# Kernel tuning notes

Measured on AMD Instinct MI355X. Metric: run time of the kernel, lower is better.

Reference implementation:

```python
import jax, jax.numpy as jnp
import numpy as np

N_SAMPLES = 2 ** 15            # 32768
N_FRAMES = N_SAMPLES // 256    # 128 (window 512, step 256)
N_EVENTS = 8
N_HARM = 8
TOTAL_COEFFS = N_SAMPLES // 2 + 1
NOISE_SPEC = 16
NYQUIST = 22050.0 / 2.0
MAX_F = 3000.0 / NYQUIST
MIN_F = 20.0 / NYQUIST
F_SPAN = MAX_F - MIN_F
Y = 20 + NOISE_SPEC + N_FRAMES + N_HARM   # 172
DIM = Y + 128 + 128                        # 428
BATCH = 16


def lin_interp(x, out_size):
    # torch F.interpolate(mode='linear', align_corners=False) along last dim
    n = x.shape[-1]
    scale = n / out_size
    coords = jnp.clip((jnp.arange(out_size) + 0.5) * scale - 0.5, 0.0, n - 1.0)
    lo = jnp.floor(coords).astype(jnp.int32)
    hi = jnp.minimum(lo + 1, n - 1)
    w = (coords - lo).astype(x.dtype)
    return x[..., lo] * (1.0 - w) + x[..., hi] * w


def setup_inputs() -> dict:
    key = jax.random.key(0)
    k1, k2 = jax.random.split(key)
    x = jax.random.normal(k1, (BATCH, N_EVENTS, DIM), dtype=jnp.float32)
    noise = jax.random.uniform(k2, (BATCH, N_EVENTS, N_SAMPLES), dtype=jnp.float32)
    return {"x": x, "noise": noise}


def reference(x, noise):
    B = x.shape[0]
    x = jax.nn.sigmoid(x)
    means = x[..., 0:1]
    stds = x[..., 1:2] * 0.1
    amps = x[..., 2:3] ** 2
    f0 = x[..., 3:4] ** 2
    factors = 1.0 + x[..., 4:12] * 7.0
    mags = (x[..., 12:20] * 0.9999) ** 2
    noise_coeff = x[..., 20:20 + NOISE_SPEC]
    fine_env = x[..., 36:36 + N_FRAMES] * 2.0 - 1.0
    amp_factors = x[..., 164:172] ** 2
    f0_var = x[..., 172:300]

    # fine amplitude envelope: cumsum over frames, clamp, upsample
    fe = jnp.clip(jnp.cumsum(fine_env.reshape(-1, N_FRAMES), axis=-1), 0.0, 1.0)
    fe = lin_interp(fe, N_SAMPLES).reshape(B, N_EVENTS, N_SAMPLES)

    # localized band-limited noise, gaussian time window
    rng = jnp.arange(N_SAMPLES, dtype=x.dtype)
    mu = jnp.clip(means * N_SAMPLES, -(N_SAMPLES // 2), N_SAMPLES * 1.5)
    sigma = jnp.clip((1e-8 + stds) * N_SAMPLES, 0.0, N_SAMPLES - 1.0)
    z = (rng - mu) / sigma                                   # (B,E,S)
    probs = jnp.exp(-0.5 * z * z) / (sigma * np.sqrt(2.0 * np.pi))
    probs = probs / (jnp.max(jnp.abs(probs), axis=-1, keepdims=True) + 1e-12)
    u = noise * 2.0 - 1.0                                    # uniform(-1,1)
    spec_shape = lin_interp(noise_coeff, TOTAL_COEFFS)       # (B,E,total_coeffs)
    ns = jnp.fft.rfft(u, axis=-1, norm='ortho') * spec_shape
    nz = jnp.fft.irfft(ns, n=N_SAMPLES, axis=-1, norm='ortho')
    atoms = probs * nz * amps * fe                           # (B,E,S)

    # harmonic resonance
    f0f = f0.reshape(-1, 1)                                  # (BE,1)
    var = f0_var.reshape(-1, N_FRAMES) * (f0f * 0.01)        # (BE,F)
    f0t = lin_interp(f0f + var, N_SAMPLES)                   # (BE,S)
    f0t = MIN_F + f0t * F_SPAN
    f0t = jnp.where(f0t > 1.0, 0.0, f0t)
    fac = factors.reshape(-1, N_HARM).at[:, 0].set(1.0)      # (BE,H)
    freqs = f0t[:, None, :] * fac[:, :, None] * np.pi        # (BE,H,S)
    osc = jnp.sin(jnp.cumsum(freqs, axis=-1)) * amp_factors.reshape(-1, N_HARM, 1)
    # cumprod of a constant per frame == geometric powers
    mg = mags.reshape(-1, N_HARM, 1) ** jnp.arange(1, N_FRAMES + 1, dtype=x.dtype)
    mg = lin_interp(mg, N_SAMPLES)                           # (BE,H,S)
    res = jnp.sum(osc * mg, axis=1).reshape(B, N_EVENTS, N_SAMPLES)

    # fft convolution (zero-padded to 2S to avoid circular wrap)
    pa = jnp.pad(atoms, ((0, 0), (0, 0), (0, N_SAMPLES)))
    pr = jnp.pad(res, ((0, 0), (0, 0), (0, N_SAMPLES)))
    conv = jnp.fft.irfft(jnp.fft.rfft(pa, axis=-1) * jnp.fft.rfft(pr, axis=-1),
                         n=2 * N_SAMPLES, axis=-1)[..., :N_SAMPLES]
    return jnp.sum(conv, axis=1, keepdims=True)              # (B,1,S)
```

## Files before the change

kernel.cpp:

```cpp
#include <hip/hip_runtime.h>
#include <math.h>

#define NSAMP 32768
#define NFFT2 65536
#define NFRM 128
#define PSTRIDE 2688
#define P_FEPAIR 64
#define P_PW2 320
#define P_LQ 1344
#define P_AF 1604
#define P_END 2636
#define TWO_PI_F 6.28318530717958647692f

typedef float2 cplx;

__device__ __forceinline__ cplx cmul_(cplx a, cplx b){ return make_float2(a.x*b.x - a.y*b.y, a.x*b.y + a.y*b.x); }
__device__ __forceinline__ cplx cadd_(cplx a, cplx b){ return make_float2(a.x+b.x, a.y+b.y); }
__device__ __forceinline__ cplx csub_(cplx a, cplx b){ return make_float2(a.x-b.x, a.y-b.y); }

__device__ __forceinline__ unsigned int packbf2(float re, float im){
  unsigned int ur = __float_as_uint(re);
  unsigned int ui = __float_as_uint(im);
  ur = (ur + 0x7FFFu + ((ur>>16)&1u)) >> 16;
  ui = (ui + 0x7FFFu + ((ui>>16)&1u)) & 0xFFFF0000u;
  return ur | ui;
}

template<bool INV>
__device__ __forceinline__ void dft4_(cplx x0,cplx x1,cplx x2,cplx x3, cplx&y0,cplx&y1,cplx&y2,cplx&y3){
  cplx t0=cadd_(x0,x2), t1=csub_(x0,x2), t2=cadd_(x1,x3), t3=csub_(x1,x3);
  y0=cadd_(t0,t2); y2=csub_(t0,t2);
  cplx it3 = make_float2(-t3.y, t3.x);
  if (INV){ y1=cadd_(t1,it3); y3=csub_(t1,it3); }
  else    { y1=csub_(t1,it3); y3=cadd_(t1,it3); }
}

template<bool INV>
__device__ __forceinline__ void dft8ip_(cplx* v){
  cplx e0,e1,e2,e3,o0,o1,o2,o3;
  dft4_<INV>(v[0],v[2],v[4],v[6], e0,e1,e2,e3);
  dft4_<INV>(v[1],v[3],v[5],v[7], o0,o1,o2,o3);
  const float r = 0.70710678118654752440f;
  cplx w1 = INV ? make_float2(r, r)    : make_float2(r,-r);
  cplx w2 = INV ? make_float2(0.f,1.f) : make_float2(0.f,-1.f);
  cplx w3 = INV ? make_float2(-r,r)    : make_float2(-r,-r);
  cplx t1 = cmul_(o1,w1), t2 = cmul_(o2,w2), t3 = cmul_(o3,w3);
  v[0]=cadd_(e0,o0); v[4]=csub_(e0,o0);
  v[1]=cadd_(e1,t1); v[5]=csub_(e1,t1);
  v[2]=cadd_(e2,t2); v[6]=csub_(e2,t2);
  v[3]=cadd_(e3,t3); v[7]=csub_(e3,t3);
}

template<bool INV>
__device__ __forceinline__ void dft16ip_(cplx* v){
  cplx t0[4], t1[4], t2[4], t3[4];
  dft4_<INV>(v[0], v[4], v[8],  v[12], t0[0],t0[1],t0[2],t0[3]);
  dft4_<INV>(v[1], v[5], v[9],  v[13], t1[0],t1[1],t1[2],t1[3]);
  dft4_<INV>(v[2], v[6], v[10], v[14], t2[0],t2[1],t2[2],t2[3]);
  dft4_<INV>(v[3], v[7], v[11], v[15], t3[0],t3[1],t3[2],t3[3]);
  const float C1=0.92387953251128675613f, S1=0.38268343236508977172f, R2=0.70710678118654752440f;
  #define TWD_(x, cc, ss) (INV ? cmul_((x), make_float2((cc), (ss))) : cmul_((x), make_float2((cc), -(ss))))
  t1[1] = TWD_(t1[1], C1, S1);
  t1[2] = TWD_(t1[2], R2, R2);
  t1[3] = TWD_(t1[3], S1, C1);
  t2[1] = TWD_(t2[1], R2, R2);
  t2[2] = TWD_(t2[2], 0.f, 1.f);
  t2[3] = TWD_(t2[3], -R2, R2);
  t3[1] = TWD_(t3[1], S1, C1);
  t3[2] = TWD_(t3[2], -R2, R2);
  t3[3] = TWD_(t3[3], -C1, -S1);
  #undef TWD_
  dft4_<INV>(t0[0], t1[0], t2[0], t3[0], v[0], v[4], v[8],  v[12]);
  dft4_<INV>(t0[1], t1[1], t2[1], t3[1], v[1], v[5], v[9],  v[13]);
  dft4_<INV>(t0[2], t1[2], t2[2], t3[2], v[2], v[6], v[10], v[14]);
  dft4_<INV>(t0[3], t1[3], t2[3], t3[3], v[3], v[7], v[11], v[15]);
}

template<int R0, bool INV>
__device__ __forceinline__ void fft_core(float* lre, float* lim, int t){
  constexpr int Q = R0/16;
  constexpr int S1 = R0 + 8;
  int g = t >> 4, a = t & 15;
  cplx v[Q];
  #pragma unroll
  for (int bb=0;bb<Q;bb++){ int idx = g*S1 + a + 16*bb; v[bb]=make_float2(lre[idx],lim[idx]); }
  if constexpr (Q==16) dft16ip_<INV>(v); else dft8ip_<INV>(v);
  float th = (INV?TWO_PI_F:-TWO_PI_F)*(float)a/(float)R0;
  float sn,cs; __sincosf(th,&sn,&cs);
  cplx w1=make_float2(cs,sn), wu=w1;
  #pragma unroll
  for (int c=1;c<Q;c++){ v[c]=cmul_(v[c],wu); wu=cmul_(wu,w1); }
  __syncthreads();
  #pragma unroll
  for (int c=0;c<Q;c++){ int m = a*Q + ((c+a)&(Q-1)); lre[g*S1+m]=v[c].x; lim[g*S1+m]=v[c].y; }
  __syncthreads();
}

template<int R0, bool INV>
__device__ __forceinline__ bool fft_stage2(const float* lre, const float* lim, int t, int& g2, int& c2, cplx* z){
  constexpr int Q = R0/16; constexpr int S1 = R0+8;
  bool active = (R0==256) || (t < 16*Q);
  g2 = (R0==256)?(t>>4):(t>>3);
  c2 = (R0==256)?(t&15):(t&7);
  if (active){
    #pragma unroll
    for (int a2=0;a2<16;a2++){ int m = a2*Q + ((c2+a2)&(Q-1)); z[a2]=make_float2(lre[g2*S1+m], lim[g2*S1+m]); }
    dft16ip_<INV>(z);
  }
  return active;
}

__global__ __launch_bounds__(256) void k_fft_pack_fwd1(const float* __restrict__ noise, cplx* __restrict__ dst, float interBase){
  constexpr int Q=16, S1=264;
  __shared__ float lre[4352], lim[4352];
  int t=threadIdx.x;
  int bx=blockIdx.x;
  int sig = bx>>3;
  int tBase=(bx&7)*16;
  const float* n0 = noise + (size_t)(2*sig)*NSAMP;
  const float* n1 = noise + (size_t)(2*sig+1)*NSAMP;
  #pragma unroll
  for (int i=0;i<16;i++){
    int e=t+256*i, g=e&15, r=e>>4;
    int ts = tBase+g+128*r;
    lre[g*S1+r]=n0[ts]*2.f-1.f;
    lim[g*S1+r]=n1[ts]*2.f-1.f;
  }
  __syncthreads();
  fft_core<256,false>(lre,lim,t);
  int g2,c2; cplx z[16];
  fft_stage2<256,false>(lre,lim,t,g2,c2,z);
  int p=tBase+g2;
  float thp=interBase*(float)p;
  float snc,csc; __sincosf(thp*(float)c2,&snc,&csc);
  float sns,css; __sincosf(thp*(float)Q,&sns,&css);
  cplx wu=make_float2(csc,snc), ws=make_float2(css,sns);
  cplx* db = dst + (size_t)sig*NSAMP;
  size_t ob=(size_t)256*(size_t)p+(size_t)c2;
  #pragma unroll
  for (int d=0;d<16;d++){ db[ob+(size_t)(d*16)]=cmul_(z[d],wu); wu=cmul_(wu,ws); }
}

__device__ __forceinline__ void fft128_natural(float* re, float* im, int t){
  __syncthreads();
  fft_core<128,false>(re,im,t);
  int g2,c2; cplx z[16];
  bool act = fft_stage2<128,false>(re,im,t,g2,c2,z);
  __syncthreads();
  if (act){
    #pragma unroll
    for (int d=0;d<16;d++){ int u=c2+8*d; re[u*17+g2]=z[d].x; im[u*17+g2]=z[d].y; }
  }
  __syncthreads();
}

__global__ __launch_bounds__(256) void k_nfilter_ip1(const cplx* __restrict__ src, cplx* __restrict__ dst,
    const float* __restrict__ P){
  __shared__ float aRe[2176], aIm[2176], bRe[2176], bIm[2176];
  __shared__ float fRe[2176], fIm[2176];
  __shared__ float c1s[16], c2sh[16];
  int t=threadIdx.x, pb=blockIdx.x, j=blockIdx.y;
  const cplx* sb = src + ((size_t)j<<15);
  cplx* db = dst + ((size_t)j<<15);
  if (t<16) c1s[t] = P[(size_t)(2*j)*PSTRIDE+28+t];
  else if (t<32) c2sh[t-16] = P[(size_t)(2*j+1)*PSTRIDE+28+(t-16)];
  #pragma unroll
  for (int i=0;i<8;i++){
    int e=t+256*i, g=e&15, r=e>>4;
    int col = (pb<8)? (pb*16+g) : (g*16);
    cplx v = sb[col + (r<<8)];
    aRe[g*136+r]=v.x; aIm[g*136+r]=v.y;
  }
  fft128_natural(aRe,aIm,t);
  if (pb<8){
    #pragma unroll
    for (int i=0;i<8;i++){
      int e=t+256*i, g=e&15, r=e>>4;
      int col = 240-pb*16+g;
      cplx v = sb[col + (r<<8)];
      bRe[g*136+r]=v.x; bIm[g*136+r]=v.y;
    }
    fft128_natural(bRe,bIm,t);
  }
  const float inv32768 = 1.0f/32768.0f;
  if (pb<8){
    for (int s=0;s<2;s++){
      __syncthreads();
      #pragma unroll
      for (int uu=0; uu<8; uu++){
        int g=t&15, u=(t>>4)+16*uu;
        if (g!=0){
          int colK = s? (240-pb*16+g) : (pb*16+g);
          int gm=16-g, um=127-u;
          float Zkx,Zky,Zmx,Zmy;
          if (s==0){ Zkx=aRe[u*17+g]; Zky=aIm[u*17+g]; Zmx=bRe[um*17+gm]; Zmy=bIm[um*17+gm]; }
          else     { Zkx=bRe[u*17+g]; Zky=bIm[u*17+g]; Zmx=aRe[um*17+gm]; Zmy=aIm[um*17+gm]; }
          int k = colK + (u<<8);
          int kb = min(k, NSAMP-k);
          float coords=fminf(fmaxf((kb+0.5f)*(16.0f/16385.0f)-0.5f,0.0f),15.0f);
          int lo=(int)coords; float w=coords-lo; int hi=min(lo+1,15);
          float s1=(c1s[lo]+w*(c1s[hi]-c1s[lo]))*inv32768;
          float s2=(c2sh[lo]+w*(c2sh[hi]-c2sh[lo]))*inv32768;
          float U1x=0.5f*(Zkx+Zmx), U1y=0.5f*(Zky-Zmy);
          float U2x=0.5f*(Zky+Zmy), U2y=-0.5f*(Zkx-Zmx);
          fRe[g*136+u]=U1x*s1 - U2y*s2; fIm[g*136+u]=U1y*s1 + U2x*s2;
        }
      }
      __syncthreads();
      fft_core<128,true>(fRe,fIm,t);
      int gg,cc; cplx z[16];
      bool act = fft_stage2<128,true>(fRe,fIm,t,gg,cc,z);
      if (act && gg!=0){
        int p = (s==0) ? (pb*16+gg) : (240-pb*16+gg);
        float thp=(TWO_PI_F/32768.0f)*(float)p;
        float snc,csc; __sincosf(thp*(float)cc,&snc,&csc);
        float sns,css; __sincosf(thp*8.0f,&sns,&css);
        cplx wu=make_float2(csc,snc), wsx=make_float2(css,sns);
        int ob=128*p+cc;
        #pragma unroll
        for (int d=0;d<16;d++){ db[ob+8*d]=cmul_(z[d],wu); wu=cmul_(wu,wsx); }
      }
    }
  } else {
    __syncthreads();
    #pragma unroll
    for (int uu=0; uu<8; uu++){
      int g=t&15, u=(t>>4)+16*uu;
      int k = g*16 + (u<<8);
      int gm=(16-g)&15;
      int um=(g==0)? ((128-u)&127) : (127-u);
      float Zkx=aRe[u*17+g], Zky=aIm[u*17+g];
      float Zmx=aRe[um*17+gm], Zmy=aIm[um*17+gm];
      int kb = min(k, NSAMP-k);
      float coords=fminf(fmaxf((kb+0.5f)*(16.0f/16385.0f)-0.5f,0.0f),15.0f);
      int lo=(int)coords; float w=coords-lo; int hi=min(lo+1,15);
      float s1=(c1s[lo]+w*(c1s[hi]-c1s[lo]))*inv32768;
      float s2=(c2sh[lo]+w*(c2sh[hi]-c2sh[lo]))*inv32768;
      float U1x=0.5f*(Zkx+Zmx), U1y=0.5f*(Zky-Zmy);
      float U2x=0.5f*(Zky+Zmy), U2y=-0.5f*(Zkx-Zmx);
      fRe[g*136+u]=U1x*s1 - U2y*s2; fIm[g*136+u]=U1y*s1 + U2x*s2;
    }
    __syncthreads();
    fft_core<128,true>(fRe,fIm,t);
    int gg,cc; cplx z[16];
    bool act = fft_stage2<128,true>(fRe,fIm,t,gg,cc,z);
    if (act){
      int p = 16*gg;
      float thp=(TWO_PI_F/32768.0f)*(float)p;
      float snc,csc; __sincosf(thp*(float)cc,&snc,&csc);
      float sns,css; __sincosf(thp*8.0f,&sns,&css);
      cplx wu=make_float2(csc,snc), wsx=make_float2(css,sns);
      int ob=128*p+cc;
      #pragma unroll
      for (int d=0;d<16;d++){ db[ob+8*d]=cmul_(z[d],wu); wu=cmul_(wu,wsx); }
    }
  }
}

__global__ __launch_bounds__(256) void k_ifinal_split(const cplx* __restrict__ src, float* __restrict__ dstf){
  constexpr int S1=264;
  __shared__ float lre[4352], lim[4352];
  int t=threadIdx.x; int bx=blockIdx.x;
  int sig=bx>>3; int tBase=(bx&7)*16;
  const cplx* sb = src + (size_t)sig*NSAMP;
  #pragma unroll
  for (int i=0;i<16;i++){
    int e=t+256*i, g=e&15, r=e>>4;
    cplx vv = sb[tBase+g + (size_t)r*128];
    lre[g*S1+r]=vv.x; lim[g*S1+r]=vv.y;
  }
  __syncthreads();
  fft_core<256,true>(lre,lim,t);
  int g2,c2; cplx z[16];
  fft_stage2<256,true>(lre,lim,t,g2,c2,z);
  __syncthreads();
  #pragma unroll
  for (int d=0;d<16;d++){ int u=c2+16*d; lre[u*17+g2]=z[d].x; lim[u*17+g2]=z[d].y; }
  __syncthreads();
  float* p0 = dstf + (size_t)(2*sig)*NSAMP;
  float* p1 = dstf + (size_t)(2*sig+1)*NSAMP;
  #pragma unroll
  for (int i=0;i<16;i++){
    int e=t+256*i, g3=e&15, u=e>>4;
    int ts = tBase+g3+u*128;
    p0[ts]=lre[u*17+g3]; p1[ts]=lim[u*17+g3];
  }
}

__global__ __launch_bounds__(256) void k_conv_build_fwd1(const float* __restrict__ P,
    const float* __restrict__ NZf, unsigned int* __restrict__ dst, int rowBase, float interBase){
  constexpr int Q=16, S1=264;
  __shared__ float smem[8448];
  float* lre = smem;
  float* lim = smem + 4224;
  float* sTab = smem;
  int t=threadIdx.x;
  int row = rowBase + blockIdx.y;
  int tBase = blockIdx.x*16;
  const float* Pr = P + (size_t)row*PSTRIDE;
  for (int i=t; i<P_END; i+=256) sTab[i] = Pr[i];
  __syncthreads();
  float mu=sTab[0], sigma=sTab[1], amp=sTab[2], pscale=sTab[3];
  float fac[8], mh[8];
  #pragma unroll
  for (int h=0;h<8;h++){ fac[h]=sTab[4+h]; mh[h]=sTab[12+h]; }
  const float2* fe2 = (const float2*)&sTab[P_FEPAIR];
  const float*  pw2 = &sTab[P_PW2];
  const float2* LQt = (const float2*)&sTab[P_LQ];
  const float*  Af  = &sTab[P_AF];
  const float* nzrow = NZf + (size_t)row*NSAMP;
  float vre[8], vim[8];
  #pragma unroll
  for (int i=0;i<8;i++){
    int e=t+256*i, g=e&15, r=e>>4;
    int ts = tBase + g + (r<<8);
    float cc=fminf(fmaxf((ts+0.5f)*(1.0f/256.0f)-0.5f,0.0f),127.0f);
    int lo=(int)cc; float w=cc-lo;
    float2 fp = fe2[lo];
    float fev = fp.x + w*fp.y;
    int slot, n0;
    if (ts<128){ slot=0; n0=ts+1; } else { int km=(ts-128)>>8; slot=km+1; n0=ts-127-(km<<8); }
    float nf=(float)n0, nf2=nf*nf;
    float2 lq = LQt[slot];
    float base = nf*lq.x + nf2*lq.y;
    float wm = (lo<127)? w : 0.0f;
    float resv=0.f;
    #pragma unroll
    for (int h=0;h<8;h++){
      float mgb = pw2[h*128+lo];
      if (mgb > 1e-7f){
        float rr = Af[slot*8+h] + fac[h]*base;
        float fr = rr - floorf(rr);
        float s = __builtin_amdgcn_sinf(fr);
        resv += s*mgb*(1.0f + wm*(mh[h]-1.0f));
      }
    }
    float zz=((float)ts-mu)/sigma;
    float prb=pscale*__expf(-0.5f*zz*zz);
    vre[i] = prb*nzrow[ts]*amp*fev;
    vim[i] = resv;
  }
  __syncthreads();
  #pragma unroll
  for (int i=0;i<8;i++){
    int e=t+256*i, g=e&15, r=e>>4;
    lre[g*S1+r]=vre[i]; lim[g*S1+r]=vim[i];
  }
  #pragma unroll
  for (int i=8;i<16;i++){
    int e=t+256*i, g=e&15, r=e>>4;
    lre[g*S1+r]=0.f; lim[g*S1+r]=0.f;
  }
  __syncthreads();
  fft_core<256,false>(lre,lim,t);
  int g2,c2; cplx z[16];
  fft_stage2<256,false>(lre,lim,t,g2,c2,z);
  int p = tBase+g2;
  float thp = interBase*(float)p;
  float snc,csc; __sincosf(thp*(float)c2,&snc,&csc);
  float sns,css; __sincosf(thp*(float)Q,&sns,&css);
  cplx wu=make_float2(csc,snc), ws=make_float2(css,sns);
  unsigned int* db = dst + (size_t)blockIdx.y*NFFT2;
  size_t ob=(size_t)256*(size_t)p+(size_t)c2;
  #pragma unroll
  for (int d=0; d<16; d++){
    cplx val = cmul_(z[d],wu);
    db[ob+(size_t)(d*16)] = packbf2(val.x, val.y);
    wu=cmul_(wu,ws);
  }
}

__global__ __launch_bounds__(256) void k_sq_inv1(const unsigned int* __restrict__ C,
    cplx* __restrict__ E0, cplx* __restrict__ E1){
  constexpr int Q=16, S1=264;
  __shared__ float lre[4352], lim[4352];
  int t=threadIdx.x;
  int tBase = blockIdx.x*16;
  int bLoc = blockIdx.y;
  int half = blockIdx.z;
  cplx* Eh = half ? E1 : E0;
  float accx[16], accy[16];
  #pragma unroll
  for (int d=0;d<16;d++){ accx[d]=0.f; accy[d]=0.f; }
  int g2=t>>4, c2=t&15;
  for (int e=0;e<4;e++){
    int sigLoc = bLoc*8 + half*4 + e;
    const unsigned int* sb = C + (size_t)sigLoc*NFFT2;
    __syncthreads();
    #pragma unroll
    for (int i=0;i<16;i++){
      int ee=t+256*i, g=ee&15, r=ee>>4;
      unsigned int u = sb[tBase+g + (size_t)r*256];
      lre[g*S1+r]=__uint_as_float(u<<16);
      lim[g*S1+r]=__uint_as_float(u & 0xFFFF0000u);
    }
    __syncthreads();
    fft_core<256,false>(lre,lim,t);
    int gg,cc; cplx z[16];
    fft_stage2<256,false>(lre,lim,t,gg,cc,z);
    #pragma unroll
    for (int d=0;d<16;d++){
      float x=z[d].x, y=z[d].y;
      accx[d] += x*x - y*y;
      accy[d] += 2.f*x*y;
    }
  }
  __syncthreads();
  const float s = 1.0f/131072.0f;
  #pragma unroll
  for (int d=0;d<16;d++){
    int rrow = c2 + 16*d;
    lre[g2*S1+rrow] = accx[d]*s;
    lim[g2*S1+rrow] = accy[d]*s;
  }
  __syncthreads();
  fft_core<256,true>(lre,lim,t);
  int gg,cc; cplx z[16];
  fft_stage2<256,true>(lre,lim,t,gg,cc,z);
  int p = tBase+gg;
  float thp = (TWO_PI_F/65536.0f)*(float)p;
  float snc,csc; __sincosf(thp*(float)cc,&snc,&csc);
  float sns,css; __sincosf(thp*(float)Q,&sns,&css);
  cplx wu=make_float2(csc,snc), ws=make_float2(css,sns);
  cplx* db = Eh + (size_t)bLoc*NFFT2;
  size_t ob=(size_t)256*(size_t)p+(size_t)cc;
  #pragma unroll
  for (int d=0; d<16; d++){ db[ob+(size_t)(d*16)]=cmul_(z[d],wu); wu=cmul_(wu,ws); }
}

__global__ __launch_bounds__(256) void k_final_imout(const cplx* __restrict__ E0, const cplx* __restrict__ E1,
    float* __restrict__ out, int batchBase){
  constexpr int S1=264;
  __shared__ float lre[4352], lim[4352];
  int t=threadIdx.x; int bx=blockIdx.x;
  int sig=bx>>4; int tBase=(bx&15)*16;
  const cplx* s0 = E0 + (size_t)sig*NFFT2;
  const cplx* s1 = E1 + (size_t)sig*NFFT2;
  #pragma unroll
  for (int i=0;i<16;i++){
    int e=t+256*i, g=e&15, r=e>>4;
    size_t idx = tBase+g+(size_t)r*256;
    cplx a=s0[idx], b=s1[idx];
    lre[g*S1+r]=a.x+b.x; lim[g*S1+r]=a.y+b.y;
  }
  __syncthreads();
  fft_core<256,true>(lre,lim,t);
  int g2,c2; cplx z[16];
  fft_stage2<256,true>(lre,lim,t,g2,c2,z);
  __syncthreads();
  #pragma unroll
  for (int d=0;d<16;d++){ int u=c2+16*d; lre[u*17+g2]=z[d].y; }
  __syncthreads();
  float* o = out + (size_t)(batchBase+sig)*NSAMP;
  #pragma unroll
  for (int i=0;i<8;i++){
    int e=t+256*i, g3=e&15, u=e>>4;
    o[tBase+g3 + u*256] = lre[u*17+g3];
  }
}

__global__ __launch_bounds__(256) void k_params(const float* __restrict__ x, float* __restrict__ P){
  int row = blockIdx.x; int t = threadIdx.x;
  const float* xr = x + row*428;
  float* Pr = P + (size_t)row*PSTRIDE;
  __shared__ float sx[428];
  __shared__ float fes[128], f0s[128];
  __shared__ double Cds[128];
  __shared__ float facs[8], ms[8], afs[8];
  __shared__ float f0_sh;
  for (int i=t;i<428;i+=256) sx[i]=1.0f/(1.0f+expf(-xr[i]));
  __syncthreads();
  if (t==0){
    float mean = sx[0]; float stds = sx[1]*0.1f; float amp = sx[2]*sx[2];
    float mu = fminf(fmaxf(mean*32768.0f, -16384.0f), 49152.0f);
    float sigma = fminf(fmaxf((1e-8f + stds)*32768.0f, 0.0f), 32767.0f);
    float c = 1.0f/(sigma*2.5066282746310002f);
    float tt0 = fminf(fmaxf(floorf(mu), 0.0f), 32767.0f);
    float tt1 = fminf(fmaxf(ceilf(mu), 0.0f), 32767.0f);
    float z0 = (tt0-mu)/sigma, z1=(tt1-mu)/sigma;
    float gmax = fmaxf(expf(-0.5f*z0*z0), expf(-0.5f*z1*z1));
    float pscale = c / (c*gmax + 1e-12f);
    Pr[0]=mu; Pr[1]=sigma; Pr[2]=amp; Pr[3]=pscale;
  }
  if (t<8){
    float fv = (t==0)?1.0f:(1.0f+sx[4+t]*7.0f);
    facs[t]=fv; Pr[4+t]=fv;
    float m = sx[12+t]*0.9999f; m=m*m; ms[t]=m; Pr[12+t]=m;
    afs[t]=sx[164+t]*sx[164+t];
  }
  if (t>=32&&t<48) Pr[28+(t-32)] = sx[20+(t-32)];
  if (t==64) f0_sh = sx[3]*sx[3];
  if (t==65){
    float acc=0.f;
    for (int f=0;f<128;f++){ acc += sx[36+f]*2.0f-1.0f; fes[f]=fminf(fmaxf(acc,0.f),1.f); }
  }
  __syncthreads();
  if (t<128){
    float f0=f0_sh;
    f0s[t] = f0 + sx[172+t]*(f0*0.01f);
  }
  __syncthreads();
  if (t==0){
    double acc = 128.0*(double)f0s[0]; Cds[0]=acc;
    for (int k=0;k<127;k++){ acc += 128.0*((double)f0s[k]+(double)f0s[k+1]); Cds[k+1]=acc; }
  }
  if (t<128){
    float v=fes[t], vh=fes[min(t+1,127)];
    Pr[P_FEPAIR+2*t]=v; Pr[P_FEPAIR+2*t+1]=vh-v;
  }
  if (t>=128 && t<136){
    int h=t-128; float m=ms[h];
    float acc = afs[h]*m;
    float* dstp = Pr + P_PW2 + h*128;
    dstp[0]=acc;
    for (int f=1;f<128;f++){ acc*=m; dstp[f]=acc; }
  }
  __syncthreads();
  const double MINF_D=20.0/11025.0, FSPAN_D=2980.0/11025.0;
  if (t<129){
    int k=t-1;
    float Lb, Qb;
    if (k<0){ Lb=(float)(0.5*(MINF_D+FSPAN_D*(double)f0s[0])); Qb=0.f; }
    else {
      double f0k=(double)f0s[k];
      double d=(k<127)?((double)f0s[k+1]-f0k):0.0;
      Lb=(float)(0.5*(MINF_D+FSPAN_D*f0k));
      Qb=(float)(0.5*FSPAN_D*d*(1.0/512.0));
    }
    Pr[P_LQ+2*t]=Lb; Pr[P_LQ+2*t+1]=Qb;
  }
  for (int idx=t; idx<129*8; idx+=256){
    int jj=idx>>3, h=idx&7, k=jj-1;
    float Aval;
    if (k<0) Aval=0.f;
    else {
      double phi0=(double)(128+256*k)*MINF_D+FSPAN_D*Cds[k];
      Aval=(float)(0.5*fmod((double)facs[h]*phi0,2.0));
    }
    Pr[P_AF+idx]=Aval;
  }
}

extern "C" void kernel_launch(void* const* d_in, const int* in_sizes, int n_in,
                              void* d_out, int out_size, void* d_ws, size_t ws_size,
                              hipStream_t stream){
  const float* x = (const float*)d_in[0];
  const float* noise = (const float*)d_in[1];
  float* out = (float*)d_out;
  char* ws = (char*)d_ws;

  const size_t szN = (size_t)64*NSAMP*sizeof(cplx);
  const size_t szE = (size_t)16*NFFT2*sizeof(cplx);
  const size_t oA  = (size_t)2<<20;
  const size_t oB  = oA + szN;
  const size_t oE0 = oB + szN;
  const size_t oE1 = oE0 + szE;
  const size_t oC  = oE1 + szE;

  const int cand[5] = {1,2,4,8,16};
  int nchunk = -1;
  for (int ci=0; ci<5; ci++){
    size_t csz = ((size_t)(128/cand[ci]))*NFFT2*sizeof(unsigned int);
    if (oC + csz <= ws_size){ nchunk = cand[ci]; break; }
  }
  if (nchunk < 0) return;
  int sigPerChunk = 128/nchunk;
  int bpc = sigPerChunk/8;

  float* P = (float*)(ws);
  cplx* A = (cplx*)(ws + oA);
  cplx* B = (cplx*)(ws + oB);
  cplx* E0 = (cplx*)(ws + oE0);
  cplx* E1 = (cplx*)(ws + oE1);
  unsigned int* C = (unsigned int*)(ws + oC);

  k_params<<<128, 256, 0, stream>>>(x, P);
  k_fft_pack_fwd1<<<512, 256, 0, stream>>>(noise, A, -TWO_PI_F/32768.0f);
  k_nfilter_ip1<<<dim3(9,64), 256, 0, stream>>>(A, B, P);
  k_ifinal_split<<<512, 256, 0, stream>>>(B, (float*)A);

  for (int c=0; c<nchunk; c++){
    int rowBase = c*sigPerChunk;
    int batchBase = c*bpc;
    k_conv_build_fwd1<<<dim3(16, sigPerChunk), 256, 0, stream>>>(P, (float*)A, C, rowBase, -TWO_PI_F/65536.0f);
    k_sq_inv1<<<dim3(16, bpc, 2), 256, 0, stream>>>(C, E0, E1);
    k_final_imout<<<bpc*16, 256, 0, stream>>>(E0, E1, out, batchBase);
  }
}
```

Baseline: 116.1 us.

## Store FFT intermediates as bf16 and split inverse accumulation into quarters

Intermediate spectra from the noise forward FFT, the filtered noise time signal, and the per-quarter partial inverse spectra are now stored as packed bf16 instead of fp32 complex. The aim is to cut global memory traffic between kernels. The squaring/inverse kernel now splits the 8 events into 4 groups of 2 instead of 2 groups of 4, doubling its grid for more parallelism. The final kernel sums four bf16 partials instead of two fp32 ones. This trades accuracy for bandwidth, with bf16 rounding applied at several extra points.

```diff
diff --git a/kernel.cpp b/kernel.cpp
--- a/kernel.cpp
+++ b/kernel.cpp
@@ -25,6 +25,13 @@
   ui = (ui + 0x7FFFu + ((ui>>16)&1u)) & 0xFFFF0000u;
   return ur | ui;
 }
+__device__ __forceinline__ float ubf_lo(unsigned int u){ return __uint_as_float(u<<16); }
+__device__ __forceinline__ float ubf_hi(unsigned int u){ return __uint_as_float(u & 0xFFFF0000u); }
+__device__ __forceinline__ unsigned short packbf1(float v){
+  unsigned int u=__float_as_uint(v);
+  return (unsigned short)((u + 0x7FFFu + ((u>>16)&1u))>>16);
+}
+__device__ __forceinline__ float unpackbf1(unsigned short s){ return __uint_as_float(((unsigned int)s)<<16); }
 
 template<bool INV>
 __device__ __forceinline__ void dft4_(cplx x0,cplx x1,cplx x2,cplx x3, cplx&y0,cplx&y1,cplx&y2,cplx&y3){
@@ -110,7 +117,7 @@
   return active;
 }
 
-__global__ __launch_bounds__(256) void k_fft_pack_fwd1(const float* __restrict__ noise, cplx* __restrict__ dst, float interBase){
+__global__ __launch_bounds__(256) void k_fft_pack_fwd1(const float* __restrict__ noise, unsigned int* __restrict__ dst, float interBase){
   constexpr int Q=16, S1=264;
   __shared__ float lre[4352], lim[4352];
   int t=threadIdx.x;
@@ -135,10 +142,14 @@
   float snc,csc; __sincosf(thp*(float)c2,&snc,&csc);
   float sns,css; __sincosf(thp*(float)Q,&sns,&css);
   cplx wu=make_float2(csc,snc), ws=make_float2(css,sns);
-  cplx* db = dst + (size_t)sig*NSAMP;
+  unsigned int* db = dst + (size_t)sig*NSAMP;
   size_t ob=(size_t)256*(size_t)p+(size_t)c2;
   #pragma unroll
-  for (int d=0;d<16;d++){ db[ob+(size_t)(d*16)]=cmul_(z[d],wu); wu=cmul_(wu,ws); }
+  for (int d=0;d<16;d++){
+    cplx val = cmul_(z[d],wu);
+    db[ob+(size_t)(d*16)] = packbf2(val.x, val.y);
+    wu=cmul_(wu,ws);
+  }
 }
 
 __device__ __forceinline__ void fft128_natural(float* re, float* im, int t){
@@ -154,13 +165,13 @@
   __syncthreads();
 }
 
-__global__ __launch_bounds__(256) void k_nfilter_ip1(const cplx* __restrict__ src, cplx* __restrict__ dst,
+__global__ __launch_bounds__(256) void k_nfilter_ip1(const unsigned int* __restrict__ src, cplx* __restrict__ dst,
     const float* __restrict__ P){
   __shared__ float aRe[2176], aIm[2176], bRe[2176], bIm[2176];
   __shared__ float fRe[2176], fIm[2176];
   __shared__ float c1s[16], c2sh[16];
   int t=threadIdx.x, pb=blockIdx.x, j=blockIdx.y;
-  const cplx* sb = src + ((size_t)j<<15);
+  const unsigned int* sb = src + ((size_t)j<<15);
   cplx* db = dst + ((size_t)j<<15);
   if (t<16) c1s[t] = P[(size_t)(2*j)*PSTRIDE+28+t];
   else if (t<32) c2sh[t-16] = P[(size_t)(2*j+1)*PSTRIDE+28+(t-16)];
@@ -168,8 +179,8 @@
   for (int i=0;i<8;i++){
     int e=t+256*i, g=e&15, r=e>>4;
     int col = (pb<8)? (pb*16+g) : (g*16);
-    cplx v = sb[col + (r<<8)];
-    aRe[g*136+r]=v.x; aIm[g*136+r]=v.y;
+    unsigned int u = sb[col + (r<<8)];
+    aRe[g*136+r]=ubf_lo(u); aIm[g*136+r]=ubf_hi(u);
   }
   fft128_natural(aRe,aIm,t);
   if (pb<8){
@@ -177,8 +188,8 @@
     for (int i=0;i<8;i++){
       int e=t+256*i, g=e&15, r=e>>4;
       int col = 240-pb*16+g;
-      cplx v = sb[col + (r<<8)];
-      bRe[g*136+r]=v.x; bIm[g*136+r]=v.y;
+      unsigned int u = sb[col + (r<<8)];
+      bRe[g*136+r]=ubf_lo(u); bIm[g*136+r]=ubf_hi(u);
     }
     fft128_natural(bRe,bIm,t);
   }
@@ -257,7 +268,7 @@
   }
 }
 
-__global__ __launch_bounds__(256) void k_ifinal_split(const cplx* __restrict__ src, float* __restrict__ dstf){
+__global__ __launch_bounds__(256) void k_ifinal_split(const cplx* __restrict__ src, unsigned short* __restrict__ dsth){
   constexpr int S1=264;
   __shared__ float lre[4352], lim[4352];
   int t=threadIdx.x; int bx=blockIdx.x;
@@ -277,18 +288,18 @@
   #pragma unroll
   for (int d=0;d<16;d++){ int u=c2+16*d; lre[u*17+g2]=z[d].x; lim[u*17+g2]=z[d].y; }
   __syncthreads();
-  float* p0 = dstf + (size_t)(2*sig)*NSAMP;
-  float* p1 = dstf + (size_t)(2*sig+1)*NSAMP;
+  unsigned short* p0 = dsth + (size_t)(2*sig)*NSAMP;
+  unsigned short* p1 = dsth + (size_t)(2*sig+1)*NSAMP;
   #pragma unroll
   for (int i=0;i<16;i++){
     int e=t+256*i, g3=e&15, u=e>>4;
     int ts = tBase+g3+u*128;
-    p0[ts]=lre[u*17+g3]; p1[ts]=lim[u*17+g3];
+    p0[ts]=packbf1(lre[u*17+g3]); p1[ts]=packbf1(lim[u*17+g3]);
   }
 }
 
 __global__ __launch_bounds__(256) void k_conv_build_fwd1(const float* __restrict__ P,
-    const float* __restrict__ NZf, unsigned int* __restrict__ dst, int rowBase, float interBase){
+    const unsigned short* __restrict__ NZh, unsigned int* __restrict__ dst, int rowBase, float interBase){
   constexpr int Q=16, S1=264;
   __shared__ float smem[8448];
   float* lre = smem;
@@ -308,7 +319,7 @@
   const float*  pw2 = &sTab[P_PW2];
   const float2* LQt = (const float2*)&sTab[P_LQ];
   const float*  Af  = &sTab[P_AF];
-  const float* nzrow = NZf + (size_t)row*NSAMP;
+  const unsigned short* nzrow = NZh + (size_t)row*NSAMP;
   float vre[8], vim[8];
   #pragma unroll
   for (int i=0;i<8;i++){
@@ -337,7 +348,7 @@
     }
     float zz=((float)ts-mu)/sigma;
     float prb=pscale*__expf(-0.5f*zz*zz);
-    vre[i] = prb*nzrow[ts]*amp*fev;
+    vre[i] = prb*unpackbf1(nzrow[ts])*amp*fev;
     vim[i] = resv;
   }
   __syncthreads();
@@ -371,28 +382,27 @@
 }
 
 __global__ __launch_bounds__(256) void k_sq_inv1(const unsigned int* __restrict__ C,
-    cplx* __restrict__ E0, cplx* __restrict__ E1){
+    unsigned int* __restrict__ E, int bpc){
   constexpr int Q=16, S1=264;
   __shared__ float lre[4352], lim[4352];
   int t=threadIdx.x;
   int tBase = blockIdx.x*16;
   int bLoc = blockIdx.y;
-  int half = blockIdx.z;
-  cplx* Eh = half ? E1 : E0;
+  int quarter = blockIdx.z;
   float accx[16], accy[16];
   #pragma unroll
   for (int d=0;d<16;d++){ accx[d]=0.f; accy[d]=0.f; }
   int g2=t>>4, c2=t&15;
-  for (int e=0;e<4;e++){
-    int sigLoc = bLoc*8 + half*4 + e;
+  for (int e=0;e<2;e++){
+    int sigLoc = bLoc*8 + quarter*2 + e;
     const unsigned int* sb = C + (size_t)sigLoc*NFFT2;
     __syncthreads();
     #pragma unroll
     for (int i=0;i<16;i++){
       int ee=t+256*i, g=ee&15, r=ee>>4;
       unsigned int u = sb[tBase+g + (size_t)r*256];
-      lre[g*S1+r]=__uint_as_float(u<<16);
-      lim[g*S1+r]=__uint_as_float(u & 0xFFFF0000u);
+      lre[g*S1+r]=ubf_lo(u);
+      lim[g*S1+r]=ubf_hi(u);
     }
     __syncthreads();
     fft_core<256,false>(lre,lim,t);
@@ -422,26 +432,31 @@
   float snc,csc; __sincosf(thp*(float)cc,&snc,&csc);
   float sns,css; __sincosf(thp*(float)Q,&sns,&css);
   cplx wu=make_float2(csc,snc), ws=make_float2(css,sns);
-  cplx* db = Eh + (size_t)bLoc*NFFT2;
+  unsigned int* db = E + ((size_t)quarter*bpc + bLoc)*NFFT2;
   size_t ob=(size_t)256*(size_t)p+(size_t)cc;
   #pragma unroll
-  for (int d=0; d<16; d++){ db[ob+(size_t)(d*16)]=cmul_(z[d],wu); wu=cmul_(wu,ws); }
-}
-
-__global__ __launch_bounds__(256) void k_final_imout(const cplx* __restrict__ E0, const cplx* __restrict__ E1,
-    float* __restrict__ out, int batchBase){
+  for (int d=0; d<16; d++){
+    cplx val = cmul_(z[d],wu);
+    db[ob+(size_t)(d*16)] = packbf2(val.x, val.y);
+    wu=cmul_(wu,ws);
+  }
+}
+
+__global__ __launch_bounds__(256) void k_final_imout(const unsigned int* __restrict__ E,
+    float* __restrict__ out, int batchBase, int bpc){
   constexpr int S1=264;
   __shared__ float lre[4352], lim[4352];
   int t=threadIdx.x; int bx=blockIdx.x;
   int sig=bx>>4; int tBase=(bx&15)*16;
-  const cplx* s0 = E0 + (size_t)sig*NFFT2;
-  const cplx* s1 = E1 + (size_t)sig*NFFT2;
+  const unsigned int* s0 = E + (size_t)sig*NFFT2;
+  size_t qstride = (size_t)bpc*NFFT2;
   #pragma unroll
   for (int i=0;i<16;i++){
     int e=t+256*i, g=e&15, r=e>>4;
     size_t idx = tBase+g+(size_t)r*256;
-    cplx a=s0[idx], b=s1[idx];
-    lre[g*S1+r]=a.x+b.x; lim[g*S1+r]=a.y+b.y;
+    unsigned int u0=s0[idx], u1=s0[qstride+idx], u2=s0[2*qstride+idx], u3=s0[3*qstride+idx];
+    lre[g*S1+r]=ubf_lo(u0)+ubf_lo(u1)+ubf_lo(u2)+ubf_lo(u3);
+    lim[g*S1+r]=ubf_hi(u0)+ubf_hi(u1)+ubf_hi(u2)+ubf_hi(u3);
   }
   __syncthreads();
   fft_core<256,true>(lre,lim,t);
@@ -549,13 +564,13 @@
   float* out = (float*)d_out;
   char* ws = (char*)d_ws;
 
-  const size_t szN = (size_t)64*NSAMP*sizeof(cplx);
-  const size_t szE = (size_t)16*NFFT2*sizeof(cplx);
+  const size_t szA = (size_t)64*NSAMP*sizeof(unsigned int);
+  const size_t szB = (size_t)64*NSAMP*sizeof(cplx);
+  const size_t szE = (size_t)4*16*NFFT2*sizeof(unsigned int);
   const size_t oA  = (size_t)2<<20;
-  const size_t oB  = oA + szN;
-  const size_t oE0 = oB + szN;
-  const size_t oE1 = oE0 + szE;
-  const size_t oC  = oE1 + szE;
+  const size_t oB  = oA + szA;
+  const size_t oE  = oB + szB;
+  const size_t oC  = oE + szE;
 
   const int cand[5] = {1,2,4,8,16};
   int nchunk = -1;
@@ -568,22 +583,21 @@
   int bpc = sigPerChunk/8;
 
   float* P = (float*)(ws);
-  cplx* A = (cplx*)(ws + oA);
+  unsigned int* A = (unsigned int*)(ws + oA);
   cplx* B = (cplx*)(ws + oB);
-  cplx* E0 = (cplx*)(ws + oE0);
-  cplx* E1 = (cplx*)(ws + oE1);
+  unsigned int* E = (unsigned int*)(ws + oE);
   unsigned int* C = (unsigned int*)(ws + oC);
 
   k_params<<<128, 256, 0, stream>>>(x, P);
   k_fft_pack_fwd1<<<512, 256, 0, stream>>>(noise, A, -TWO_PI_F/32768.0f);
   k_nfilter_ip1<<<dim3(9,64), 256, 0, stream>>>(A, B, P);
-  k_ifinal_split<<<512, 256, 0, stream>>>(B, (float*)A);
+  k_ifinal_split<<<512, 256, 0, stream>>>(B, (unsigned short*)A);
 
   for (int c=0; c<nchunk; c++){
     int rowBase = c*sigPerChunk;
     int batchBase = c*bpc;
-    k_conv_build_fwd1<<<dim3(16, sigPerChunk), 256, 0, stream>>>(P, (float*)A, C, rowBase, -TWO_PI_F/65536.0f);
-    k_sq_inv1<<<dim3(16, bpc, 2), 256, 0, stream>>>(C, E0, E1);
-    k_final_imout<<<bpc*16, 256, 0, stream>>>(E0, E1, out, batchBase);
-  }
-}
+    k_conv_build_fwd1<<<dim3(16, sigPerChunk), 256, 0, stream>>>(P, (unsigned short*)A, C, rowBase, -TWO_PI_F/65536.0f);
+    k_sq_inv1<<<dim3(16, bpc, 4), 256, 0, stream>>>(C, E, bpc);
+    k_final_imout<<<bpc*16, 256, 0, stream>>>(E, out, batchBase, bpc);
+  }
+}
```

Measured after the change: 117.6 us. No clear change (+1.3%).
